# Performance work log

Measured on AMD Instinct MI355X. Metric: run time of the kernel, lower is better.

## Reference

```python
import jax, jax.numpy as jnp
import numpy as np

N_NODES = 50000


def _glorot(key, fan_in, fan_out):
    lim = jnp.sqrt(6.0 / (fan_in + fan_out)).astype(jnp.float32)
    return jax.random.uniform(key, (fan_in, fan_out), jnp.float32, -lim, lim)


def gcn_layer(x, W, b, src, dst, deg_inv_sqrt):
    # PyG GCNConv: x' = D^{-1/2} (A + I) D^{-1/2} (x W) + b
    h = x @ W  # [N, F_out]
    norm = deg_inv_sqrt[src] * deg_inv_sqrt[dst]  # [E+N]
    msg = norm[:, None] * h[src]                  # gather + scale
    out = jax.ops.segment_sum(msg, dst, num_segments=x.shape[0])
    return out + b


def setup_inputs() -> dict:
    key = jax.random.key(0)
    ks = jax.random.split(key, 8)
    in_c, out_c = 128, 64
    hid = 2 * out_c
    x = jax.random.normal(ks[0], (N_NODES, in_c), jnp.float32)
    edge_index = jax.random.randint(ks[1], (2, 800000), 0, N_NODES, jnp.int64)
    return {
        "x": x,
        "edge_index": edge_index,
        "W1": _glorot(ks[2], in_c, hid), "b1": jnp.zeros((hid,), jnp.float32),
        "W2": _glorot(ks[3], hid, hid),  "b2": jnp.zeros((hid,), jnp.float32),
        "W3": _glorot(ks[4], hid, out_c), "b3": jnp.zeros((out_c,), jnp.float32),
    }


def reference(x, edge_index, W1, b1, W2, b2, W3, b3):
    n = x.shape[0]
    loops = jnp.arange(n, dtype=edge_index.dtype)
    src = jnp.concatenate([edge_index[0], loops])  # [E+N]
    dst = jnp.concatenate([edge_index[1], loops])
    deg = jax.ops.segment_sum(jnp.ones_like(dst, dtype=x.dtype), dst, num_segments=n)
    deg_inv_sqrt = jnp.where(deg > 0, jax.lax.rsqrt(deg), 0.0)

    h = jax.nn.relu(gcn_layer(x, W1, b1, src, dst, deg_inv_sqrt))
    h = jax.nn.relu(gcn_layer(h, W2, b2, src, dst, deg_inv_sqrt))
    return gcn_layer(h, W3, b3, src, dst, deg_inv_sqrt)
```

## Files before the change

kernel.cpp:

```cpp
#include <hip/hip_runtime.h>
#include <hip/hip_bf16.h>
#include <hip/hip_fp16.h>
#include <cstdint>
#include <cstddef>

typedef _Float16 half8_t __attribute__((ext_vector_type(8)));
typedef float f32x4 __attribute__((ext_vector_type(4)));
typedef unsigned short ushort8_v __attribute__((ext_vector_type(8)));


__global__ __launch_bounds__(256) void prep_kernel(int* __restrict__ cnt, int N4,
                                                   const float* __restrict__ W1, _Float16* __restrict__ wt1,
                                                   const float* __restrict__ W2, _Float16* __restrict__ wt2,
                                                   const float* __restrict__ W3, _Float16* __restrict__ wt3,
                                                   _Float16* __restrict__ gA, _Float16* __restrict__ gB,
                                                   _Float16* __restrict__ gC, int N) {
  int i = blockIdx.x * 256 + threadIdx.x;
  if (i < N4) {
    *(int4*)&cnt[i * 4] = make_int4(0, 0, 0, 0);
    return;
  }
  int j = i - N4;
  if (j < 16384) {
    int k = j >> 7, c = j & 127;
    wt1[c * 128 + k] = (_Float16)W1[j];
    return;
  }
  j -= 16384;
  if (j < 16384) {
    int k = j >> 7, c = j & 127;
    wt2[c * 128 + k] = (_Float16)W2[j];
    return;
  }
  j -= 16384;
  if (j < 8192) {
    int k = j >> 6, c = j & 63;
    wt3[c * 128 + k] = (_Float16)W3[j];
    return;
  }
  j -= 8192;
  if (j < 40) {
    half8_t z = {};
    if (j < 16)       *(half8_t*)&gA[(size_t)N * 128 + j * 8] = z;
    else if (j < 32)  *(half8_t*)&gB[(size_t)N * 128 + (j - 16) * 8] = z;
    else              *(half8_t*)&gC[(size_t)N * 64 + (j - 32) * 8] = z;
  }
}


__global__ __launch_bounds__(256) void countpos_fill_kernel(const int* __restrict__ dst,
                                                            int* __restrict__ cnt,
                                                            ushort* __restrict__ pos, int E,
                                                            int* __restrict__ ssInt, int ssInts,
                                                            int countBlocks, int fillPat) {
  if (blockIdx.x >= countBlocks) {
    int f = ((blockIdx.x - countBlocks) * 256 + threadIdx.x) * 4;
    if (f + 4 <= ssInts) *(int4*)&ssInt[f] = make_int4(fillPat, fillPat, fillPat, fillPat);
    else for (; f < ssInts; ++f) ssInt[f] = fillPat;
    return;
  }
  int e = (blockIdx.x * blockDim.x + threadIdx.x) * 4;
  if (e + 4 <= E) {
    int4 d = *(const int4*)&dst[e];
    int p0 = atomicAdd(&cnt[d.x], 1);
    int p1 = atomicAdd(&cnt[d.y], 1);
    int p2 = atomicAdd(&cnt[d.z], 1);
    int p3 = atomicAdd(&cnt[d.w], 1);
    ushort4 pk;
    pk.x = (ushort)p0; pk.y = (ushort)p1; pk.z = (ushort)p2; pk.w = (ushort)p3;
    *(ushort4*)&pos[e] = pk;
  } else {
    for (; e < E; ++e) pos[e] = (ushort)atomicAdd(&cnt[dst[e]], 1);
  }
}

__global__ __launch_bounds__(256) void block_sum_kernel(const int* __restrict__ cnt,
                                                        int* __restrict__ bsum, int N) {
  const int tid = threadIdx.x, lane = tid & 63, wid = tid >> 6;
  __shared__ int wt[4];
  int base = blockIdx.x * 2048 + tid * 8;
  int s = 0;
#pragma unroll
  for (int q = 0; q < 8; ++q) { int i = base + q; if (i < N) s += (cnt[i] + 7) & ~7; }
#pragma unroll
  for (int off = 32; off; off >>= 1) s += __shfl_down(s, off);
  if (lane == 0) wt[wid] = s;
  __syncthreads();
  if (tid == 0) bsum[blockIdx.x] = wt[0] + wt[1] + wt[2] + wt[3];
}

__global__ __launch_bounds__(256) void scan_bsum_kernel(const int* __restrict__ bsum,
                                                        int* __restrict__ boff,
                                                        int NB, int* __restrict__ rpN) {
  __shared__ int sh[256];
  const int tid = threadIdx.x;
  int v = (tid < NB) ? bsum[tid] : 0;
  sh[tid] = v;
  __syncthreads();
  for (int off = 1; off < 256; off <<= 1) {
    int t = (tid >= off) ? sh[tid - off] : 0;
    __syncthreads();
    sh[tid] += t;
    __syncthreads();
  }
  if (tid < NB) boff[tid] = sh[tid] - v;
  if (tid == 255) rpN[0] = sh[255];
}

__global__ __launch_bounds__(256) void scan_apply_kernel(const int* __restrict__ cnt,
                                                         const int* __restrict__ boff,
                                                         int* __restrict__ rp,
                                                         float* __restrict__ dis, int N) {
  const int tid = threadIdx.x, lane = tid & 63, wid = tid >> 6;
  __shared__ int wtot[4], wexc[4];
  int base = blockIdx.x * 2048 + tid * 8;
  int v[8]; int s = 0;
#pragma unroll
  for (int q = 0; q < 8; ++q) {
    int i = base + q; int x = (i < N) ? cnt[i] : 0;
    v[q] = x; s += (x + 7) & ~7;
  }
  int sc = s;
#pragma unroll
  for (int off = 1; off < 64; off <<= 1) { int t = __shfl_up(sc, off); if (lane >= off) sc += t; }
  if (lane == 63) wtot[wid] = sc;
  __syncthreads();
  if (tid == 0) { int r = 0; for (int wq = 0; wq < 4; ++wq) { wexc[wq] = r; r += wtot[wq]; } }
  __syncthreads();
  int thr = boff[blockIdx.x] + wexc[wid] + (sc - s);
#pragma unroll
  for (int q = 0; q < 8; ++q) {
    int i = base + q;
    if (i < N) { rp[i] = thr; dis[i] = rsqrtf((float)(v[q] + 1)); }
    thr += (v[q] + 7) & ~7;
  }
}


__global__ __launch_bounds__(256) void place_gemm1_kernel(const int* __restrict__ src,
                                                          const int* __restrict__ dst,
                                                          const ushort* __restrict__ pos,
                                                          const int* __restrict__ rp,
                                                          ushort* __restrict__ ss, int E,
                                                          const float* __restrict__ X,
                                                          const half8_t* __restrict__ Wt,
                                                          const float* __restrict__ dis,
                                                          _Float16* __restrict__ G, int N,
                                                          int gemmBlocks) {
  if (blockIdx.x >= gemmBlocks) {
    int e = ((blockIdx.x - gemmBlocks) * blockDim.x + threadIdx.x) * 4;
    if (e + 4 <= E) {
      int4 d = *(const int4*)&dst[e];
      ushort4 p = *(const ushort4*)&pos[e];
      int4 s = *(const int4*)&src[e];
      int r0 = rp[d.x], r1 = rp[d.y], r2 = rp[d.z], r3 = rp[d.w];
      ss[r0 + p.x] = (ushort)s.x;
      ss[r1 + p.y] = (ushort)s.y;
      ss[r2 + p.z] = (ushort)s.z;
      ss[r3 + p.w] = (ushort)s.w;
    } else {
      for (; e < E; ++e) ss[rp[dst[e]] + pos[e]] = (ushort)src[e];
    }
    return;
  }
  const int wave = threadIdx.x >> 6;
  const int lane = threadIdx.x & 63;
  const int wm = wave >> 1, wn = wave & 1;
  const int row0 = blockIdx.x * 128 + wm * 64;
  const int col0 = wn * 64;
  const int lr = lane & 15;
  const int lk = lane >> 4;
  f32x4 acc[4][4];
#pragma unroll
  for (int r = 0; r < 4; ++r)
#pragma unroll
    for (int c = 0; c < 4; ++c) acc[r][c] = (f32x4){0.f, 0.f, 0.f, 0.f};

#pragma unroll
  for (int ks = 0; ks < 4; ++ks) {
    half8_t a[4], b[4];
#pragma unroll
    for (int r = 0; r < 4; ++r) {
      int row = row0 + r * 16 + lr;
      half8_t av = {};
      if (row < N) {
        const float* xp = &X[(size_t)row * 128 + ks * 32 + lk * 8];
        float4 xa = *(const float4*)xp;
        float4 xb = *(const float4*)(xp + 4);
        av[0] = (_Float16)xa.x; av[1] = (_Float16)xa.y; av[2] = (_Float16)xa.z; av[3] = (_Float16)xa.w;
        av[4] = (_Float16)xb.x; av[5] = (_Float16)xb.y; av[6] = (_Float16)xb.z; av[7] = (_Float16)xb.w;
      }
      a[r] = av;
    }
#pragma unroll
    for (int c = 0; c < 4; ++c) {
      int col = col0 + c * 16 + lr;
      b[c] = Wt[(size_t)col * 16 + ks * 4 + lk];
    }
#pragma unroll
    for (int r = 0; r < 4; ++r)
#pragma unroll
      for (int c = 0; c < 4; ++c)
        acc[r][c] = __builtin_amdgcn_mfma_f32_16x16x32_f16(a[r], b[c], acc[r][c], 0, 0, 0);
  }

#pragma unroll
  for (int r = 0; r < 4; ++r) {
#pragma unroll
    for (int q = 0; q < 4; ++q) {
      int row = row0 + r * 16 + lk * 4 + q;
      if (row < N) {
        float dv = dis[row];
#pragma unroll
        for (int c = 0; c < 4; ++c)
          G[(size_t)row * 128 + col0 + c * 16 + lr] = (_Float16)(acc[r][c][q] * dv);
      }
    }
  }
}


template <int COUT>
__global__ __launch_bounds__(256) void fused_agg_gemm_kernel(const _Float16* __restrict__ G,
                                                             const int* __restrict__ rp,
                                                             const ushort* __restrict__ ss,
                                                             const float* __restrict__ dis,
                                                             const float* __restrict__ bias,
                                                             const half8_t* __restrict__ Wt,
                                                             _Float16* __restrict__ G2, int N) {
  __shared__ _Float16 sh[32][136];
  const int wave = threadIdx.x >> 6;
  const int lane = threadIdx.x & 63;
  const int grp = lane >> 4;
  const int sub = lane & 15;
  const int nb0 = blockIdx.x * 32;

#pragma unroll
  for (int it = 0; it < 2; ++it) {
    const int wl = it * 16 + wave * 4 + grp;
    const int w = nb0 + wl;
    if (w < N) {
      const int e0 = rp[w], e1 = rp[w + 1];
      float acc[8];
      half8_t sv = *(const half8_t*)&G[(size_t)w * 128 + sub * 8];
#pragma unroll
      for (int j = 0; j < 8; ++j) acc[j] = (float)sv[j];
      for (int e = e0; e < e1; e += 8) {
        ushort8_v iv = *(const ushort8_v*)&ss[e];
        half8_t v[8];
#pragma unroll
        for (int q = 0; q < 8; ++q) v[q] = *(const half8_t*)&G[(size_t)iv[q] * 128 + sub * 8];
#pragma unroll
        for (int j = 0; j < 8; ++j)
          acc[j] += (((float)v[0][j] + (float)v[1][j]) + ((float)v[2][j] + (float)v[3][j])) +
                    (((float)v[4][j] + (float)v[5][j]) + ((float)v[6][j] + (float)v[7][j]));
      }
      float d = dis[w];
      float4 b0 = *(const float4*)&bias[sub * 8];
      float4 b1 = *(const float4*)&bias[sub * 8 + 4];
      float bb[8] = {b0.x, b0.y, b0.z, b0.w, b1.x, b1.y, b1.z, b1.w};
      half8_t o;
#pragma unroll
      for (int j = 0; j < 8; ++j) {
        float v = fmaxf(d * acc[j] + bb[j], 0.f);
        o[j] = (_Float16)v;
      }
      *(half8_t*)&sh[wl][sub * 8] = o;
    }
  }
  __syncthreads();

  const int lr = lane & 15;
  const int lk = lane >> 4;
  constexpr int NC = COUT / 64;
  const int col0 = wave * (COUT / 4);
  f32x4 acc2[2][NC];
#pragma unroll
  for (int r = 0; r < 2; ++r)
#pragma unroll
    for (int c = 0; c < NC; ++c) acc2[r][c] = (f32x4){0.f, 0.f, 0.f, 0.f};

#pragma unroll
  for (int ks = 0; ks < 4; ++ks) {
    half8_t a[2], b[NC];
#pragma unroll
    for (int r = 0; r < 2; ++r)
      a[r] = *(const half8_t*)&sh[r * 16 + lr][ks * 32 + lk * 8];
#pragma unroll
    for (int c = 0; c < NC; ++c) {
      int col = col0 + c * 16 + lr;
      b[c] = Wt[(size_t)col * 16 + ks * 4 + lk];
    }
#pragma unroll
    for (int r = 0; r < 2; ++r)
#pragma unroll
      for (int c = 0; c < NC; ++c)
        acc2[r][c] = __builtin_amdgcn_mfma_f32_16x16x32_f16(a[r], b[c], acc2[r][c], 0, 0, 0);
  }

#pragma unroll
  for (int r = 0; r < 2; ++r) {
#pragma unroll
    for (int q = 0; q < 4; ++q) {
      int row = nb0 + r * 16 + lk * 4 + q;
      if (row < N) {
        float dv = dis[row];
#pragma unroll
        for (int c = 0; c < NC; ++c)
          G2[(size_t)row * COUT + col0 + c * 16 + lr] = (_Float16)(acc2[r][c][q] * dv);
      }
    }
  }
}


__global__ __launch_bounds__(256) void agg64_kernel(const _Float16* __restrict__ G,
                                                    const int* __restrict__ rp,
                                                    const ushort* __restrict__ ss,
                                                    const float* __restrict__ dis,
                                                    const float* __restrict__ bias,
                                                    float* __restrict__ OUT, int N) {
  const int wave = threadIdx.x >> 6;
  const int lane = threadIdx.x & 63;
  const int grp = lane >> 3;
  const int sub = lane & 7;
  const int w = blockIdx.x * 32 + wave * 8 + grp;
  if (w >= N) return;
  const int e0 = rp[w], e1 = rp[w + 1];
  float acc[8];
  half8_t sv = *(const half8_t*)&G[(size_t)w * 64 + sub * 8];
#pragma unroll
  for (int j = 0; j < 8; ++j) acc[j] = (float)sv[j];
  for (int e = e0; e < e1; e += 8) {
    ushort8_v iv = *(const ushort8_v*)&ss[e];
    half8_t v[8];
#pragma unroll
    for (int q = 0; q < 8; ++q) v[q] = *(const half8_t*)&G[(size_t)iv[q] * 64 + sub * 8];
#pragma unroll
    for (int j = 0; j < 8; ++j)
      acc[j] += (((float)v[0][j] + (float)v[1][j]) + ((float)v[2][j] + (float)v[3][j])) +
                (((float)v[4][j] + (float)v[5][j]) + ((float)v[6][j] + (float)v[7][j]));
  }
  float d = dis[w];
  float4 b0 = *(const float4*)&bias[sub * 8];
  float4 b1 = *(const float4*)&bias[sub * 8 + 4];
  float4 o0, o1;
  o0.x = d * acc[0] + b0.x; o0.y = d * acc[1] + b0.y;
  o0.z = d * acc[2] + b0.z; o0.w = d * acc[3] + b0.w;
  o1.x = d * acc[4] + b1.x; o1.y = d * acc[5] + b1.y;
  o1.z = d * acc[6] + b1.z; o1.w = d * acc[7] + b1.w;
  *(float4*)&OUT[(size_t)w * 64 + sub * 8] = o0;
  *(float4*)&OUT[(size_t)w * 64 + sub * 8 + 4] = o1;
}


extern "C" void kernel_launch(void* const* d_in, const int* in_sizes, int n_in,
                              void* d_out, int out_size, void* d_ws, size_t ws_size,
                              hipStream_t stream) {
  const float* x  = (const float*)d_in[0];
  const int*   ei = (const int*)d_in[1];
  const float* W1 = (const float*)d_in[2];
  const float* b1 = (const float*)d_in[3];
  const float* W2 = (const float*)d_in[4];
  const float* b2 = (const float*)d_in[5];
  const float* W3 = (const float*)d_in[6];
  const float* b3 = (const float*)d_in[7];

  const int inC = in_sizes[2] / in_sizes[3];
  const int N = in_sizes[0] / inC;
  const int E = in_sizes[1] / 2;

  const int SSPAD = ((E + 7 * N + 8) + 7) & ~7;

  auto align256 = [](size_t v) { return (v + 255) & ~(size_t)255; };
  char* p = (char*)d_ws;
  int* cnt = (int*)p;   p += align256((size_t)N * 4);
  int* rp  = (int*)p;   p += align256((size_t)(N + 1) * 4);
  ushort* ss = (ushort*)p;  p += align256((size_t)SSPAD * 2);
  ushort* pos = (ushort*)p; p += align256((size_t)E * 2);
  float* dis = (float*)p; p += align256((size_t)N * 4);
  _Float16* gA = (_Float16*)p; p += align256((size_t)(N + 1) * 128 * 2);
  _Float16* gB = (_Float16*)p; p += align256((size_t)(N + 1) * 128 * 2);
  _Float16* gC = (_Float16*)p; p += align256((size_t)(N + 1) * 64 * 2);
  _Float16* wt1 = (_Float16*)p; p += align256((size_t)128 * 128 * 2);
  _Float16* wt2 = (_Float16*)p; p += align256((size_t)128 * 128 * 2);
  _Float16* wt3 = (_Float16*)p; p += align256((size_t)64 * 128 * 2);
  int* bsum = (int*)p;  p += align256(1024 * 4);
  int* boff = (int*)p;  p += align256(1024 * 4);

  const int* srcv = ei;
  const int* dstv = ei + E;

  const int NB = (N + 2047) / 2048;
  const int eB4 = (E / 4 + 255) / 256;
  const int N4 = (N + 3) / 4;
  const int prepTot = N4 + 16384 + 16384 + 8192 + 40;
  const int ssInts = SSPAD / 2;
  const int fillB = (ssInts / 4 + 255) / 256;
  const int fillPat = (int)(((unsigned)N) | (((unsigned)N) << 16));

  prep_kernel<<<(prepTot + 255) / 256, 256, 0, stream>>>(cnt, N4, W1, wt1, W2, wt2, W3, wt3,
                                                         gA, gB, gC, N);
  countpos_fill_kernel<<<eB4 + fillB, 256, 0, stream>>>(dstv, cnt, pos, E,
                                                        (int*)ss, ssInts, eB4, fillPat);
  block_sum_kernel<<<NB, 256, 0, stream>>>(cnt, bsum, N);
  scan_bsum_kernel<<<1, 256, 0, stream>>>(bsum, boff, NB, rp + N);
  scan_apply_kernel<<<NB, 256, 0, stream>>>(cnt, boff, rp, dis, N);

  const int g1B = (N + 127) / 128;
  const int fB  = (N + 31) / 32;
  const int a64B = (N + 31) / 32;

  place_gemm1_kernel<<<g1B + eB4, 256, 0, stream>>>(srcv, dstv, pos, rp, ss, E,
                                                    x, (const half8_t*)wt1, dis, gA, N, g1B);
  fused_agg_gemm_kernel<128><<<fB, 256, 0, stream>>>(gA, rp, ss, dis, b1, (const half8_t*)wt2, gB, N);
  fused_agg_gemm_kernel<64><<<fB, 256, 0, stream>>>(gB, rp, ss, dis, b2, (const half8_t*)wt3, gC, N);
  agg64_kernel<<<a64B, 256, 0, stream>>>(gC, rp, ss, dis, b3, (float*)d_out, N);
}
```

Baseline: 169.3 us.

## Unroll gather loop to 16 edges, use nontemporal loads, halve fused block rows

The gather-aggregate loops in the fused aggregate+GEMM kernels and the final 64-wide aggregation now take 16 neighbours per iteration, with an 8-edge tail, so more independent loads are in flight. Neighbour feature loads switch to nontemporal loads. The fused kernel now handles 16 nodes per block instead of 32, doubling the grid to improve load balance and occupancy, at the cost of weight-tile reuse per MFMA. The nontemporal hint may lower cache hit rates for the repeated random gathers, and the 16-wide unroll raises register pressure.

```diff
diff --git a/kernel.cpp b/kernel.cpp
--- a/kernel.cpp
+++ b/kernel.cpp
@@ -228,45 +228,61 @@
                                                              const float* __restrict__ bias,
                                                              const half8_t* __restrict__ Wt,
                                                              _Float16* __restrict__ G2, int N) {
-  __shared__ _Float16 sh[32][136];
+  __shared__ _Float16 sh[16][136];
   const int wave = threadIdx.x >> 6;
   const int lane = threadIdx.x & 63;
   const int grp = lane >> 4;
   const int sub = lane & 15;
-  const int nb0 = blockIdx.x * 32;
-
-#pragma unroll
-  for (int it = 0; it < 2; ++it) {
-    const int wl = it * 16 + wave * 4 + grp;
-    const int w = nb0 + wl;
-    if (w < N) {
-      const int e0 = rp[w], e1 = rp[w + 1];
-      float acc[8];
-      half8_t sv = *(const half8_t*)&G[(size_t)w * 128 + sub * 8];
-#pragma unroll
-      for (int j = 0; j < 8; ++j) acc[j] = (float)sv[j];
-      for (int e = e0; e < e1; e += 8) {
-        ushort8_v iv = *(const ushort8_v*)&ss[e];
-        half8_t v[8];
-#pragma unroll
-        for (int q = 0; q < 8; ++q) v[q] = *(const half8_t*)&G[(size_t)iv[q] * 128 + sub * 8];
-#pragma unroll
-        for (int j = 0; j < 8; ++j)
-          acc[j] += (((float)v[0][j] + (float)v[1][j]) + ((float)v[2][j] + (float)v[3][j])) +
-                    (((float)v[4][j] + (float)v[5][j]) + ((float)v[6][j] + (float)v[7][j]));
-      }
-      float d = dis[w];
-      float4 b0 = *(const float4*)&bias[sub * 8];
-      float4 b1 = *(const float4*)&bias[sub * 8 + 4];
-      float bb[8] = {b0.x, b0.y, b0.z, b0.w, b1.x, b1.y, b1.z, b1.w};
-      half8_t o;
-#pragma unroll
-      for (int j = 0; j < 8; ++j) {
-        float v = fmaxf(d * acc[j] + bb[j], 0.f);
-        o[j] = (_Float16)v;
-      }
-      *(half8_t*)&sh[wl][sub * 8] = o;
-    }
+  const int nb0 = blockIdx.x * 16;
+  const int wl = wave * 4 + grp;
+  const int w = nb0 + wl;
+
+  if (w < N) {
+    const int e0 = rp[w], e1 = rp[w + 1];
+    float acc[8];
+    half8_t sv = *(const half8_t*)&G[(size_t)w * 128 + sub * 8];
+#pragma unroll
+    for (int j = 0; j < 8; ++j) acc[j] = (float)sv[j];
+    int e = e0;
+    for (; e + 16 <= e1; e += 16) {
+      ushort8_v iv0 = *(const ushort8_v*)&ss[e];
+      ushort8_v iv1 = *(const ushort8_v*)&ss[e + 8];
+      half8_t v[16];
+#pragma unroll
+      for (int q = 0; q < 8; ++q)
+        v[q] = __builtin_nontemporal_load((const half8_t*)&G[(size_t)iv0[q] * 128 + sub * 8]);
+#pragma unroll
+      for (int q = 0; q < 8; ++q)
+        v[8 + q] = __builtin_nontemporal_load((const half8_t*)&G[(size_t)iv1[q] * 128 + sub * 8]);
+#pragma unroll
+      for (int j = 0; j < 8; ++j)
+        acc[j] += ((((float)v[0][j] + (float)v[1][j]) + ((float)v[2][j] + (float)v[3][j])) +
+                   (((float)v[4][j] + (float)v[5][j]) + ((float)v[6][j] + (float)v[7][j]))) +
+                  ((((float)v[8][j] + (float)v[9][j]) + ((float)v[10][j] + (float)v[11][j])) +
+                   (((float)v[12][j] + (float)v[13][j]) + ((float)v[14][j] + (float)v[15][j])));
+    }
+    if (e < e1) {
+      ushort8_v iv = *(const ushort8_v*)&ss[e];
+      half8_t v[8];
+#pragma unroll
+      for (int q = 0; q < 8; ++q)
+        v[q] = __builtin_nontemporal_load((const half8_t*)&G[(size_t)iv[q] * 128 + sub * 8]);
+#pragma unroll
+      for (int j = 0; j < 8; ++j)
+        acc[j] += (((float)v[0][j] + (float)v[1][j]) + ((float)v[2][j] + (float)v[3][j])) +
+                  (((float)v[4][j] + (float)v[5][j]) + ((float)v[6][j] + (float)v[7][j]));
+    }
+    float d = dis[w];
+    float4 b0 = *(const float4*)&bias[sub * 8];
+    float4 b1 = *(const float4*)&bias[sub * 8 + 4];
+    float bb[8] = {b0.x, b0.y, b0.z, b0.w, b1.x, b1.y, b1.z, b1.w};
+    half8_t o;
+#pragma unroll
+    for (int j = 0; j < 8; ++j) {
+      float v = fmaxf(d * acc[j] + bb[j], 0.f);
+      o[j] = (_Float16)v;
+    }
+    *(half8_t*)&sh[wl][sub * 8] = o;
   }
   __syncthreads();
 
@@ -274,41 +290,32 @@
   const int lk = lane >> 4;
   constexpr int NC = COUT / 64;
   const int col0 = wave * (COUT / 4);
-  f32x4 acc2[2][NC];
-#pragma unroll
-  for (int r = 0; r < 2; ++r)
-#pragma unroll
-    for (int c = 0; c < NC; ++c) acc2[r][c] = (f32x4){0.f, 0.f, 0.f, 0.f};
+  f32x4 acc2[NC];
+#pragma unroll
+  for (int c = 0; c < NC; ++c) acc2[c] = (f32x4){0.f, 0.f, 0.f, 0.f};
 
 #pragma unroll
   for (int ks = 0; ks < 4; ++ks) {
-    half8_t a[2], b[NC];
-#pragma unroll
-    for (int r = 0; r < 2; ++r)
-      a[r] = *(const half8_t*)&sh[r * 16 + lr][ks * 32 + lk * 8];
+    half8_t a = *(const half8_t*)&sh[lr][ks * 32 + lk * 8];
+    half8_t b[NC];
 #pragma unroll
     for (int c = 0; c < NC; ++c) {
       int col = col0 + c * 16 + lr;
       b[c] = Wt[(size_t)col * 16 + ks * 4 + lk];
     }
 #pragma unroll
-    for (int r = 0; r < 2; ++r)
+    for (int c = 0; c < NC; ++c)
+      acc2[c] = __builtin_amdgcn_mfma_f32_16x16x32_f16(a, b[c], acc2[c], 0, 0, 0);
+  }
+
+#pragma unroll
+  for (int q = 0; q < 4; ++q) {
+    int row = nb0 + lk * 4 + q;
+    if (row < N) {
+      float dv = dis[row];
 #pragma unroll
       for (int c = 0; c < NC; ++c)
-        acc2[r][c] = __builtin_amdgcn_mfma_f32_16x16x32_f16(a[r], b[c], acc2[r][c], 0, 0, 0);
-  }
-
-#pragma unroll
-  for (int r = 0; r < 2; ++r) {
-#pragma unroll
-    for (int q = 0; q < 4; ++q) {
-      int row = nb0 + r * 16 + lk * 4 + q;
-      if (row < N) {
-        float dv = dis[row];
-#pragma unroll
-        for (int c = 0; c < NC; ++c)
-          G2[(size_t)row * COUT + col0 + c * 16 + lr] = (_Float16)(acc2[r][c][q] * dv);
-      }
+        G2[(size_t)row * COUT + col0 + c * 16 + lr] = (_Float16)(acc2[c][q] * dv);
     }
   }
 }
@@ -331,11 +338,30 @@
   half8_t sv = *(const half8_t*)&G[(size_t)w * 64 + sub * 8];
 #pragma unroll
   for (int j = 0; j < 8; ++j) acc[j] = (float)sv[j];
-  for (int e = e0; e < e1; e += 8) {
+  int e = e0;
+  for (; e + 16 <= e1; e += 16) {
+    ushort8_v iv0 = *(const ushort8_v*)&ss[e];
+    ushort8_v iv1 = *(const ushort8_v*)&ss[e + 8];
+    half8_t v[16];
+#pragma unroll
+    for (int q = 0; q < 8; ++q)
+      v[q] = __builtin_nontemporal_load((const half8_t*)&G[(size_t)iv0[q] * 64 + sub * 8]);
+#pragma unroll
+    for (int q = 0; q < 8; ++q)
+      v[8 + q] = __builtin_nontemporal_load((const half8_t*)&G[(size_t)iv1[q] * 64 + sub * 8]);
+#pragma unroll
+    for (int j = 0; j < 8; ++j)
+      acc[j] += ((((float)v[0][j] + (float)v[1][j]) + ((float)v[2][j] + (float)v[3][j])) +
+                 (((float)v[4][j] + (float)v[5][j]) + ((float)v[6][j] + (float)v[7][j]))) +
+                ((((float)v[8][j] + (float)v[9][j]) + ((float)v[10][j] + (float)v[11][j])) +
+                 (((float)v[12][j] + (float)v[13][j]) + ((float)v[14][j] + (float)v[15][j])));
+  }
+  if (e < e1) {
     ushort8_v iv = *(const ushort8_v*)&ss[e];
     half8_t v[8];
 #pragma unroll
-    for (int q = 0; q < 8; ++q) v[q] = *(const half8_t*)&G[(size_t)iv[q] * 64 + sub * 8];
+    for (int q = 0; q < 8; ++q)
+      v[q] = __builtin_nontemporal_load((const half8_t*)&G[(size_t)iv[q] * 64 + sub * 8]);
 #pragma unroll
     for (int j = 0; j < 8; ++j)
       acc[j] += (((float)v[0][j] + (float)v[1][j]) + ((float)v[2][j] + (float)v[3][j])) +
@@ -408,7 +434,7 @@
   scan_apply_kernel<<<NB, 256, 0, stream>>>(cnt, boff, rp, dis, N);
 
   const int g1B = (N + 127) / 128;
-  const int fB  = (N + 31) / 32;
+  const int fB  = (N + 15) / 16;
   const int a64B = (N + 31) / 32;
 
   place_gemm1_kernel<<<g1B + eB4, 256, 0, stream>>>(srcv, dstv, pos, rp, ss, E,
```

After: 200.2 us. 1.18x slower.

## Move first-layer GEMM into count kernel and apply degree scaling afterwards

Applied to the files above, without the earlier changes.

The layer-1 X·W1 GEMM is moved out of the place kernel and into the count/fill kernel, so it runs alongside the atomic degree counting before the scan. Because the degree normalisation is not known yet at that point, the GEMM writes unscaled fp16 results. A separate elementwise pass in the place kernel then rescales each row by its inverse square root degree. This hides the GEMM behind the latency-bound atomics and scans, at the cost of an extra read-modify-write over gA and one extra fp16 rounding step.

```diff
diff --git a/kernel.cpp b/kernel.cpp
--- a/kernel.cpp
+++ b/kernel.cpp
@@ -48,31 +48,89 @@
 }
 
 
-__global__ __launch_bounds__(256) void countpos_fill_kernel(const int* __restrict__ dst,
-                                                            int* __restrict__ cnt,
-                                                            ushort* __restrict__ pos, int E,
-                                                            int* __restrict__ ssInt, int ssInts,
-                                                            int countBlocks, int fillPat) {
-  if (blockIdx.x >= countBlocks) {
+__global__ __launch_bounds__(256) void countpos_fill_gemm1_kernel(
+    const int* __restrict__ dst, int* __restrict__ cnt, ushort* __restrict__ pos, int E,
+    int* __restrict__ ssInt, int ssInts, int fillPat,
+    const float* __restrict__ X, const half8_t* __restrict__ Wt, _Float16* __restrict__ G, int N,
+    int countBlocks, int fillBlocks) {
+  if (blockIdx.x < countBlocks) {
+    int e = (blockIdx.x * blockDim.x + threadIdx.x) * 4;
+    if (e + 4 <= E) {
+      int4 d = *(const int4*)&dst[e];
+      int p0 = atomicAdd(&cnt[d.x], 1);
+      int p1 = atomicAdd(&cnt[d.y], 1);
+      int p2 = atomicAdd(&cnt[d.z], 1);
+      int p3 = atomicAdd(&cnt[d.w], 1);
+      ushort4 pk;
+      pk.x = (ushort)p0; pk.y = (ushort)p1; pk.z = (ushort)p2; pk.w = (ushort)p3;
+      *(ushort4*)&pos[e] = pk;
+    } else {
+      for (; e < E; ++e) pos[e] = (ushort)atomicAdd(&cnt[dst[e]], 1);
+    }
+    return;
+  }
+  if (blockIdx.x < countBlocks + fillBlocks) {
     int f = ((blockIdx.x - countBlocks) * 256 + threadIdx.x) * 4;
     if (f + 4 <= ssInts) *(int4*)&ssInt[f] = make_int4(fillPat, fillPat, fillPat, fillPat);
     else for (; f < ssInts; ++f) ssInt[f] = fillPat;
     return;
   }
-  int e = (blockIdx.x * blockDim.x + threadIdx.x) * 4;
-  if (e + 4 <= E) {
-    int4 d = *(const int4*)&dst[e];
-    int p0 = atomicAdd(&cnt[d.x], 1);
-    int p1 = atomicAdd(&cnt[d.y], 1);
-    int p2 = atomicAdd(&cnt[d.z], 1);
-    int p3 = atomicAdd(&cnt[d.w], 1);
-    ushort4 pk;
-    pk.x = (ushort)p0; pk.y = (ushort)p1; pk.z = (ushort)p2; pk.w = (ushort)p3;
-    *(ushort4*)&pos[e] = pk;
-  } else {
-    for (; e < E; ++e) pos[e] = (ushort)atomicAdd(&cnt[dst[e]], 1);
-  }
-}
+  const int gb = blockIdx.x - countBlocks - fillBlocks;
+  const int wave = threadIdx.x >> 6;
+  const int lane = threadIdx.x & 63;
+  const int wm = wave >> 1, wn = wave & 1;
+  const int row0 = gb * 128 + wm * 64;
+  const int col0 = wn * 64;
+  const int lr = lane & 15;
+  const int lk = lane >> 4;
+  f32x4 acc[4][4];
+#pragma unroll
+  for (int r = 0; r < 4; ++r)
+#pragma unroll
+    for (int c = 0; c < 4; ++c) acc[r][c] = (f32x4){0.f, 0.f, 0.f, 0.f};
+
+#pragma unroll
+  for (int ks = 0; ks < 4; ++ks) {
+    half8_t a[4], b[4];
+#pragma unroll
+    for (int r = 0; r < 4; ++r) {
+      int row = row0 + r * 16 + lr;
+      half8_t av = {};
+      if (row < N) {
+        const float* xp = &X[(size_t)row * 128 + ks * 32 + lk * 8];
+        float4 xa = *(const float4*)xp;
+        float4 xb = *(const float4*)(xp + 4);
+        av[0] = (_Float16)xa.x; av[1] = (_Float16)xa.y; av[2] = (_Float16)xa.z; av[3] = (_Float16)xa.w;
+        av[4] = (_Float16)xb.x; av[5] = (_Float16)xb.y; av[6] = (_Float16)xb.z; av[7] = (_Float16)xb.w;
+      }
+      a[r] = av;
+    }
+#pragma unroll
+    for (int c = 0; c < 4; ++c) {
+      int col = col0 + c * 16 + lr;
+      b[c] = Wt[(size_t)col * 16 + ks * 4 + lk];
+    }
+#pragma unroll
+    for (int r = 0; r < 4; ++r)
+#pragma unroll
+      for (int c = 0; c < 4; ++c)
+        acc[r][c] = __builtin_amdgcn_mfma_f32_16x16x32_f16(a[r], b[c], acc[r][c], 0, 0, 0);
+  }
+
+#pragma unroll
+  for (int r = 0; r < 4; ++r) {
+#pragma unroll
+    for (int q = 0; q < 4; ++q) {
+      int row = row0 + r * 16 + lk * 4 + q;
+      if (row < N) {
+#pragma unroll
+        for (int c = 0; c < 4; ++c)
+          G[(size_t)row * 128 + col0 + c * 16 + lr] = (_Float16)(acc[r][c][q]);
+      }
+    }
+  }
+}
+
 
 __global__ __launch_bounds__(256) void block_sum_kernel(const int* __restrict__ cnt,
                                                         int* __restrict__ bsum, int N) {
@@ -137,18 +195,16 @@
 }
 
 
-__global__ __launch_bounds__(256) void place_gemm1_kernel(const int* __restrict__ src,
+__global__ __launch_bounds__(256) void place_scale_kernel(const int* __restrict__ src,
                                                           const int* __restrict__ dst,
                                                           const ushort* __restrict__ pos,
                                                           const int* __restrict__ rp,
                                                           ushort* __restrict__ ss, int E,
-                                                          const float* __restrict__ X,
-                                                          const half8_t* __restrict__ Wt,
-                                                          const float* __restrict__ dis,
-                                                          _Float16* __restrict__ G, int N,
-                                                          int gemmBlocks) {
-  if (blockIdx.x >= gemmBlocks) {
-    int e = ((blockIdx.x - gemmBlocks) * blockDim.x + threadIdx.x) * 4;
+                                                          _Float16* __restrict__ gA,
+                                                          const float* __restrict__ dis, int N,
+                                                          int placeBlocks) {
+  if (blockIdx.x < placeBlocks) {
+    int e = (blockIdx.x * blockDim.x + threadIdx.x) * 4;
     if (e + 4 <= E) {
       int4 d = *(const int4*)&dst[e];
       ushort4 p = *(const ushort4*)&pos[e];
@@ -163,59 +219,15 @@
     }
     return;
   }
-  const int wave = threadIdx.x >> 6;
-  const int lane = threadIdx.x & 63;
-  const int wm = wave >> 1, wn = wave & 1;
-  const int row0 = blockIdx.x * 128 + wm * 64;
-  const int col0 = wn * 64;
-  const int lr = lane & 15;
-  const int lk = lane >> 4;
-  f32x4 acc[4][4];
-#pragma unroll
-  for (int r = 0; r < 4; ++r)
-#pragma unroll
-    for (int c = 0; c < 4; ++c) acc[r][c] = (f32x4){0.f, 0.f, 0.f, 0.f};
-
-#pragma unroll
-  for (int ks = 0; ks < 4; ++ks) {
-    half8_t a[4], b[4];
-#pragma unroll
-    for (int r = 0; r < 4; ++r) {
-      int row = row0 + r * 16 + lr;
-      half8_t av = {};
-      if (row < N) {
-        const float* xp = &X[(size_t)row * 128 + ks * 32 + lk * 8];
-        float4 xa = *(const float4*)xp;
-        float4 xb = *(const float4*)(xp + 4);
-        av[0] = (_Float16)xa.x; av[1] = (_Float16)xa.y; av[2] = (_Float16)xa.z; av[3] = (_Float16)xa.w;
-        av[4] = (_Float16)xb.x; av[5] = (_Float16)xb.y; av[6] = (_Float16)xb.z; av[7] = (_Float16)xb.w;
-      }
-      a[r] = av;
-    }
-#pragma unroll
-    for (int c = 0; c < 4; ++c) {
-      int col = col0 + c * 16 + lr;
-      b[c] = Wt[(size_t)col * 16 + ks * 4 + lk];
-    }
-#pragma unroll
-    for (int r = 0; r < 4; ++r)
-#pragma unroll
-      for (int c = 0; c < 4; ++c)
-        acc[r][c] = __builtin_amdgcn_mfma_f32_16x16x32_f16(a[r], b[c], acc[r][c], 0, 0, 0);
-  }
-
-#pragma unroll
-  for (int r = 0; r < 4; ++r) {
-#pragma unroll
-    for (int q = 0; q < 4; ++q) {
-      int row = row0 + r * 16 + lk * 4 + q;
-      if (row < N) {
-        float dv = dis[row];
-#pragma unroll
-        for (int c = 0; c < 4; ++c)
-          G[(size_t)row * 128 + col0 + c * 16 + lr] = (_Float16)(acc[r][c][q] * dv);
-      }
-    }
+  int t = (blockIdx.x - placeBlocks) * 256 + threadIdx.x;
+  int row = t >> 4;
+  if (row < N) {
+    float d = dis[row];
+    half8_t v = *(half8_t*)&gA[(size_t)row * 128 + (t & 15) * 8];
+    half8_t o;
+#pragma unroll
+    for (int j = 0; j < 8; ++j) o[j] = (_Float16)((float)v[j] * d);
+    *(half8_t*)&gA[(size_t)row * 128 + (t & 15) * 8] = o;
   }
 }
 
@@ -398,21 +410,23 @@
   const int ssInts = SSPAD / 2;
   const int fillB = (ssInts / 4 + 255) / 256;
   const int fillPat = (int)(((unsigned)N) | (((unsigned)N) << 16));
+  const int g1B = (N + 127) / 128;
+  const int scaleB = ((N * 16) + 255) / 256;
 
   prep_kernel<<<(prepTot + 255) / 256, 256, 0, stream>>>(cnt, N4, W1, wt1, W2, wt2, W3, wt3,
                                                          gA, gB, gC, N);
-  countpos_fill_kernel<<<eB4 + fillB, 256, 0, stream>>>(dstv, cnt, pos, E,
-                                                        (int*)ss, ssInts, eB4, fillPat);
+  countpos_fill_gemm1_kernel<<<eB4 + fillB + g1B, 256, 0, stream>>>(
+      dstv, cnt, pos, E, (int*)ss, ssInts, fillPat,
+      x, (const half8_t*)wt1, gA, N, eB4, fillB);
   block_sum_kernel<<<NB, 256, 0, stream>>>(cnt, bsum, N);
   scan_bsum_kernel<<<1, 256, 0, stream>>>(bsum, boff, NB, rp + N);
   scan_apply_kernel<<<NB, 256, 0, stream>>>(cnt, boff, rp, dis, N);
-
-  const int g1B = (N + 127) / 128;
+  place_scale_kernel<<<eB4 + scaleB, 256, 0, stream>>>(srcv, dstv, pos, rp, ss, E,
+                                                       gA, dis, N, eB4);
+
   const int fB  = (N + 31) / 32;
   const int a64B = (N + 31) / 32;
 
-  place_gemm1_kernel<<<g1B + eB4, 256, 0, stream>>>(srcv, dstv, pos, rp, ss, E,
-                                                    x, (const half8_t*)wt1, dis, gA, N, g1B);
   fused_agg_gemm_kernel<128><<<fB, 256, 0, stream>>>(gA, rp, ss, dis, b1, (const half8_t*)wt2, gB, N);
   fused_agg_gemm_kernel<64><<<fB, 256, 0, stream>>>(gB, rp, ss, dis, b2, (const half8_t*)wt3, gC, N);
   agg64_kernel<<<a64B, 256, 0, stream>>>(gC, rp, ss, dis, b3, (float*)d_out, N);
```

Measured after the change: 177.1 us. 1.05x slower.

## Bucket nodes by padded degree and process aggregation in degree-sorted order

Applied to the files above, without the earlier changes.

Builds a 16-bucket histogram of padded in-degree during the scan kernels and produces a permutation that groups nodes with similar degree. The aggregation kernels then walk nodes through this permutation, so lanes in a wave have similar edge-loop trip counts, which reduces divergence and load imbalance. In exchange it adds shared and global atomics in the scan stage, an extra indirection per node, and less locality in the output writes.

```diff
diff --git a/kernel.cpp b/kernel.cpp
--- a/kernel.cpp
+++ b/kernel.cpp
@@ -14,7 +14,7 @@
                                                    const float* __restrict__ W2, _Float16* __restrict__ wt2,
                                                    const float* __restrict__ W3, _Float16* __restrict__ wt3,
                                                    _Float16* __restrict__ gA, _Float16* __restrict__ gB,
-                                                   _Float16* __restrict__ gC, int N) {
+                                                   _Float16* __restrict__ gC, int* __restrict__ ghist, int N) {
   int i = blockIdx.x * 256 + threadIdx.x;
   if (i < N4) {
     *(int4*)&cnt[i * 4] = make_int4(0, 0, 0, 0);
@@ -44,7 +44,10 @@
     if (j < 16)       *(half8_t*)&gA[(size_t)N * 128 + j * 8] = z;
     else if (j < 32)  *(half8_t*)&gB[(size_t)N * 128 + (j - 16) * 8] = z;
     else              *(half8_t*)&gC[(size_t)N * 64 + (j - 32) * 8] = z;
-  }
+    return;
+  }
+  j -= 40;
+  if (j < 16) ghist[j] = 0;
 }
 
 
@@ -74,24 +77,40 @@
   }
 }
 
+
 __global__ __launch_bounds__(256) void block_sum_kernel(const int* __restrict__ cnt,
-                                                        int* __restrict__ bsum, int N) {
+                                                        int* __restrict__ bsum,
+                                                        int* __restrict__ ghist, int N) {
   const int tid = threadIdx.x, lane = tid & 63, wid = tid >> 6;
   __shared__ int wt[4];
+  __shared__ int lh[16];
+  if (tid < 16) lh[tid] = 0;
+  __syncthreads();
   int base = blockIdx.x * 2048 + tid * 8;
   int s = 0;
 #pragma unroll
-  for (int q = 0; q < 8; ++q) { int i = base + q; if (i < N) s += (cnt[i] + 7) & ~7; }
+  for (int q = 0; q < 8; ++q) {
+    int i = base + q;
+    if (i < N) {
+      int x = cnt[i];
+      s += (x + 7) & ~7;
+      int b = (x + 7) >> 3; if (b > 15) b = 15;
+      atomicAdd(&lh[b], 1);
+    }
+  }
 #pragma unroll
   for (int off = 32; off; off >>= 1) s += __shfl_down(s, off);
   if (lane == 0) wt[wid] = s;
   __syncthreads();
   if (tid == 0) bsum[blockIdx.x] = wt[0] + wt[1] + wt[2] + wt[3];
+  if (tid < 16 && lh[tid]) atomicAdd(&ghist[tid], lh[tid]);
 }
 
 __global__ __launch_bounds__(256) void scan_bsum_kernel(const int* __restrict__ bsum,
                                                         int* __restrict__ boff,
-                                                        int NB, int* __restrict__ rpN) {
+                                                        int NB, int* __restrict__ rpN,
+                                                        const int* __restrict__ ghist,
+                                                        int* __restrict__ gcur) {
   __shared__ int sh[256];
   const int tid = threadIdx.x;
   int v = (tid < NB) ? bsum[tid] : 0;
@@ -105,14 +124,22 @@
   }
   if (tid < NB) boff[tid] = sh[tid] - v;
   if (tid == 255) rpN[0] = sh[255];
+  if (tid == 0) {
+    int r = 0;
+    for (int k = 0; k < 16; ++k) { gcur[k] = r; r += ghist[k]; }
+  }
 }
 
 __global__ __launch_bounds__(256) void scan_apply_kernel(const int* __restrict__ cnt,
                                                          const int* __restrict__ boff,
                                                          int* __restrict__ rp,
-                                                         float* __restrict__ dis, int N) {
+                                                         float* __restrict__ dis,
+                                                         int* __restrict__ gcur,
+                                                         int* __restrict__ perm, int N) {
   const int tid = threadIdx.x, lane = tid & 63, wid = tid >> 6;
   __shared__ int wtot[4], wexc[4];
+  __shared__ int lh[16], lbase[16], lcur[16];
+  if (tid < 16) { lh[tid] = 0; lcur[tid] = 0; }
   int base = blockIdx.x * 2048 + tid * 8;
   int v[8]; int s = 0;
 #pragma unroll
@@ -128,11 +155,28 @@
   if (tid == 0) { int r = 0; for (int wq = 0; wq < 4; ++wq) { wexc[wq] = r; r += wtot[wq]; } }
   __syncthreads();
   int thr = boff[blockIdx.x] + wexc[wid] + (sc - s);
+  int bk[8];
 #pragma unroll
   for (int q = 0; q < 8; ++q) {
     int i = base + q;
-    if (i < N) { rp[i] = thr; dis[i] = rsqrtf((float)(v[q] + 1)); }
+    if (i < N) {
+      rp[i] = thr; dis[i] = rsqrtf((float)(v[q] + 1));
+      int b = (v[q] + 7) >> 3; if (b > 15) b = 15;
+      bk[q] = b;
+      atomicAdd(&lh[b], 1);
+    }
     thr += (v[q] + 7) & ~7;
+  }
+  __syncthreads();
+  if (tid < 16 && lh[tid]) lbase[tid] = atomicAdd(&gcur[tid], lh[tid]);
+  __syncthreads();
+#pragma unroll
+  for (int q = 0; q < 8; ++q) {
+    int i = base + q;
+    if (i < N) {
+      int r = atomicAdd(&lcur[bk[q]], 1);
+      perm[lbase[bk[q]] + r] = i;
+    }
   }
 }
 
@@ -227,6 +271,7 @@
                                                              const float* __restrict__ dis,
                                                              const float* __restrict__ bias,
                                                              const half8_t* __restrict__ Wt,
+                                                             const int* __restrict__ perm,
                                                              _Float16* __restrict__ G2, int N) {
   __shared__ _Float16 sh[32][136];
   const int wave = threadIdx.x >> 6;
@@ -238,8 +283,9 @@
 #pragma unroll
   for (int it = 0; it < 2; ++it) {
     const int wl = it * 16 + wave * 4 + grp;
-    const int w = nb0 + wl;
-    if (w < N) {
+    const int idx = nb0 + wl;
+    if (idx < N) {
+      const int w = perm[idx];
       const int e0 = rp[w], e1 = rp[w + 1];
       float acc[8];
       half8_t sv = *(const half8_t*)&G[(size_t)w * 128 + sub * 8];
@@ -302,8 +348,9 @@
   for (int r = 0; r < 2; ++r) {
 #pragma unroll
     for (int q = 0; q < 4; ++q) {
-      int row = nb0 + r * 16 + lk * 4 + q;
-      if (row < N) {
+      int idx2 = nb0 + r * 16 + lk * 4 + q;
+      if (idx2 < N) {
+        int row = perm[idx2];
         float dv = dis[row];
 #pragma unroll
         for (int c = 0; c < NC; ++c)
@@ -319,13 +366,15 @@
                                                     const ushort* __restrict__ ss,
                                                     const float* __restrict__ dis,
                                                     const float* __restrict__ bias,
+                                                    const int* __restrict__ perm,
                                                     float* __restrict__ OUT, int N) {
   const int wave = threadIdx.x >> 6;
   const int lane = threadIdx.x & 63;
   const int grp = lane >> 3;
   const int sub = lane & 7;
-  const int w = blockIdx.x * 32 + wave * 8 + grp;
-  if (w >= N) return;
+  const int idx = blockIdx.x * 32 + wave * 8 + grp;
+  if (idx >= N) return;
+  const int w = perm[idx];
   const int e0 = rp[w], e1 = rp[w + 1];
   float acc[8];
   half8_t sv = *(const half8_t*)&G[(size_t)w * 64 + sub * 8];
@@ -379,6 +428,7 @@
   ushort* ss = (ushort*)p;  p += align256((size_t)SSPAD * 2);
   ushort* pos = (ushort*)p; p += align256((size_t)E * 2);
   float* dis = (float*)p; p += align256((size_t)N * 4);
+  int* perm = (int*)p;  p += align256((size_t)N * 4);
   _Float16* gA = (_Float16*)p; p += align256((size_t)(N + 1) * 128 * 2);
   _Float16* gB = (_Float16*)p; p += align256((size_t)(N + 1) * 128 * 2);
   _Float16* gC = (_Float16*)p; p += align256((size_t)(N + 1) * 64 * 2);
@@ -387,6 +437,8 @@
   _Float16* wt3 = (_Float16*)p; p += align256((size_t)64 * 128 * 2);
   int* bsum = (int*)p;  p += align256(1024 * 4);
   int* boff = (int*)p;  p += align256(1024 * 4);
+  int* ghist = (int*)p; p += align256(16 * 4);
+  int* gcur  = (int*)p; p += align256(16 * 4);
 
   const int* srcv = ei;
   const int* dstv = ei + E;
@@ -394,18 +446,18 @@
   const int NB = (N + 2047) / 2048;
   const int eB4 = (E / 4 + 255) / 256;
   const int N4 = (N + 3) / 4;
-  const int prepTot = N4 + 16384 + 16384 + 8192 + 40;
+  const int prepTot = N4 + 16384 + 16384 + 8192 + 40 + 16;
   const int ssInts = SSPAD / 2;
   const int fillB = (ssInts / 4 + 255) / 256;
   const int fillPat = (int)(((unsigned)N) | (((unsigned)N) << 16));
 
   prep_kernel<<<(prepTot + 255) / 256, 256, 0, stream>>>(cnt, N4, W1, wt1, W2, wt2, W3, wt3,
-                                                         gA, gB, gC, N);
+                                                         gA, gB, gC, ghist, N);
   countpos_fill_kernel<<<eB4 + fillB, 256, 0, stream>>>(dstv, cnt, pos, E,
                                                         (int*)ss, ssInts, eB4, fillPat);
-  block_sum_kernel<<<NB, 256, 0, stream>>>(cnt, bsum, N);
-  scan_bsum_kernel<<<1, 256, 0, stream>>>(bsum, boff, NB, rp + N);
-  scan_apply_kernel<<<NB, 256, 0, stream>>>(cnt, boff, rp, dis, N);
+  block_sum_kernel<<<NB, 256, 0, stream>>>(cnt, bsum, ghist, N);
+  scan_bsum_kernel<<<1, 256, 0, stream>>>(bsum, boff, NB, rp + N, ghist, gcur);
+  scan_apply_kernel<<<NB, 256, 0, stream>>>(cnt, boff, rp, dis, gcur, perm, N);
 
   const int g1B = (N + 127) / 128;
   const int fB  = (N + 31) / 32;
@@ -413,7 +465,7 @@
 
   place_gemm1_kernel<<<g1B + eB4, 256, 0, stream>>>(srcv, dstv, pos, rp, ss, E,
                                                     x, (const half8_t*)wt1, dis, gA, N, g1B);
-  fused_agg_gemm_kernel<128><<<fB, 256, 0, stream>>>(gA, rp, ss, dis, b1, (const half8_t*)wt2, gB, N);
-  fused_agg_gemm_kernel<64><<<fB, 256, 0, stream>>>(gB, rp, ss, dis, b2, (const half8_t*)wt3, gC, N);
-  agg64_kernel<<<a64B, 256, 0, stream>>>(gC, rp, ss, dis, b3, (float*)d_out, N);
-}
+  fused_agg_gemm_kernel<128><<<fB, 256, 0, stream>>>(gA, rp, ss, dis, b1, (const half8_t*)wt2, perm, gB, N);
+  fused_agg_gemm_kernel<64><<<fB, 256, 0, stream>>>(gB, rp, ss, dis, b2, (const half8_t*)wt3, perm, gC, N);
+  agg64_kernel<<<a64B, 256, 0, stream>>>(gC, rp, ss, dis, b3, perm, (float*)d_out, N);
+}
```

After: 176.5 us. +4.3%, slower.
